# Kernel optimization log

Measured on AMD Instinct MI355X. Metric: run time of the kernel, lower is better.

The kernel has to match this reference:

```python
import jax, jax.numpy as jnp
import numpy as np

LN_EPS = 1e-5
NEG_INF = -1e30


def setup_inputs() -> dict:
    key = jax.random.key(0)
    ks = jax.random.split(key, 8)
    B, S, D_MODEL, Q_IN = 1, 2048, 1024, 512
    HI, DI = 16, 64            # indexer heads / head_dim
    H, DQK, DV = 8, 64, 64     # MLA heads, qk_head_dim, v_head_dim
    return {
        "x": jax.random.normal(ks[0], (B, S, D_MODEL), jnp.float32),
        "q_input": jax.random.normal(ks[1], (B, S, Q_IN), jnp.float32),
        "q": jax.random.normal(ks[2], (B, S, H, DQK), jnp.float32),
        "k": jax.random.normal(ks[3], (B, S, H, DQK), jnp.float32),
        "v": jax.random.normal(ks[4], (B, S, H, DV), jnp.float32),
        "w_q": jax.random.normal(ks[5], (Q_IN, HI * DI), jnp.float32) * (Q_IN ** -0.5),
        "w_k": jax.random.normal(ks[6], (D_MODEL, DI), jnp.float32) * (D_MODEL ** -0.5),
        "ln_g": jnp.ones((DI,), jnp.float32),
        "ln_b": jnp.zeros((DI,), jnp.float32),
        "w_weights": jax.random.normal(ks[7], (D_MODEL, HI), jnp.float32) * (D_MODEL ** -0.5),
        "top_k": 128,
    }


def _indexer_topk(x, q_input, w_q, w_k, ln_g, ln_b, w_weights, top_k):
    """Lightning indexer: per-head relevance scores -> weighted sum -> causal top-k indices."""
    B, S, _ = x.shape
    HI = w_weights.shape[1]
    DI = w_k.shape[1]
    qi = (q_input @ w_q).reshape(B, S, HI, DI)          # bqhd
    ki = x @ w_k                                         # bkd
    mu = ki.mean(-1, keepdims=True)
    var = ((ki - mu) ** 2).mean(-1, keepdims=True)
    ki = (ki - mu) * jax.lax.rsqrt(var + LN_EPS) * ln_g + ln_b
    # per-head weights; scores*w summed over h == (sum_h w*q) . k  (fused, same math)
    w = (x @ w_weights) * (HI ** -0.5)                   # bqh
    q_eff = jnp.einsum("bqhd,bqh->bqd", qi, w) * (DI ** -0.5)
    scores = jnp.einsum("bqd,bkd->bqk", q_eff, ki)       # [B,S,S]
    pos = jnp.arange(S)
    causal = jnp.where(pos[None, :] <= pos[:, None], 0.0, NEG_INF).astype(scores.dtype)
    scores = scores + causal[None]
    return jax.lax.top_k(scores, top_k)[1]               # [B,S,K]


def reference(x, q_input, q, k, v, w_q, w_k, ln_g, ln_b, w_weights, top_k):
    B, S, H, DQK = q.shape
    DV = v.shape[-1]
    idx = _indexer_topk(x, q_input, w_q, w_k, ln_g, ln_b, w_weights, top_k)  # [B,S,K]

    qh = q.transpose(0, 2, 1, 3)   # [B,H,Sq,D]
    kh = k.transpose(0, 2, 1, 3)   # [B,H,Sk,D]
    vh = v.transpose(0, 2, 1, 3)

    def gather(kv, ix):            # kv [Sk,D], ix [Sq,K] -> [Sq,K,D]
        return kv[ix]

    gather_h = jax.vmap(gather, in_axes=(0, None))       # over heads, shared idx
    gather_bh = jax.vmap(gather_h, in_axes=(0, 0))       # over batch
    k_sel = gather_bh(kh, idx)     # [B,H,Sq,K,D]
    v_sel = gather_bh(vh, idx)     # [B,H,Sq,K,Dv]

    att = jnp.einsum("bhqd,bhqkd->bhqk", qh, k_sel) * (DQK ** -0.5)
    pos = jnp.arange(S)
    valid = idx[:, None, :, :] <= pos[None, None, :, None]   # causal validity of gathered idx
    att = jnp.where(valid, att, NEG_INF)
    p = jax.nn.softmax(att, axis=-1)
    out = jnp.einsum("bhqk,bhqkd->bhqd", p, v_sel)
    return out.transpose(0, 2, 1, 3)   # [B,S,H,Dv]
```

## Files before the change

### kernel.cpp

```cpp
#include <hip/hip_runtime.h>
#include <hip/hip_bf16.h>
#include <hip/hip_fp16.h>
#include <math.h>

#define S 2048
#define DM 1024
#define QIN 512
#define HI 16
#define DI 64
#define NH 8
#define TOPK 128
#define LN_EPS 1e-5f
#define KP 8

typedef float f32x4 __attribute__((ext_vector_type(4)));
typedef short s16x8 __attribute__((ext_vector_type(8)));

__device__ __forceinline__ float wave_sum(float v){
#pragma unroll
  for (int o = 32; o; o >>= 1) v += __shfl_xor(v, o);
  return v;
}
__device__ __forceinline__ float wave_max(float v){
#pragma unroll
  for (int o = 32; o; o >>= 1) v = fmaxf(v, __shfl_xor(v, o));
  return v;
}
__device__ __forceinline__ unsigned short f2bf(float x){
  unsigned u = __float_as_uint(x);
  unsigned r = u + 0x7FFFu + ((u >> 16) & 1u);
  return (unsigned short)(r >> 16);
}
__device__ __forceinline__ float bf2f(unsigned short s){
  return __uint_as_float(((unsigned)s) << 16);
}
__device__ __forceinline__ unsigned short f2h(float x){
  return __half_as_ushort(__float2half_rn(x));
}
union UH2 { unsigned int u; __half2 h; };
__device__ __forceinline__ __half2 as_half2(unsigned int u){ UH2 x; x.u = u; return x.h; }

__global__ __launch_bounds__(256) void k_prep(const float* __restrict__ qin,
                                              unsigned short* __restrict__ Ah,
                                              unsigned short* __restrict__ Al,
                                              const float* __restrict__ k,
                                              unsigned short* __restrict__ kh,
                                              const float* __restrict__ v,
                                              unsigned short* __restrict__ vh,
                                              const float* __restrict__ wq,
                                              unsigned short* __restrict__ Bh,
                                              unsigned short* __restrict__ Bl){
  __shared__ unsigned short lh[32][33];
  __shared__ unsigned short ll[32][33];
  const int SEG0 = S * QIN / 4;
  const int SEG1 = S * NH * 64 / 4;
  const int bid = blockIdx.x;
  if (bid < 3072){
    int id = bid * 256 + threadIdx.x;
    if (id < SEG0){
      float4 f = ((const float4*)qin)[id];
      ushort4 h, lo;
      h.x = f2bf(f.x); lo.x = f2bf(f.x - bf2f(h.x));
      h.y = f2bf(f.y); lo.y = f2bf(f.y - bf2f(h.y));
      h.z = f2bf(f.z); lo.z = f2bf(f.z - bf2f(h.z));
      h.w = f2bf(f.w); lo.w = f2bf(f.w - bf2f(h.w));
      ((ushort4*)Ah)[id] = h;
      ((ushort4*)Al)[id] = lo;
    } else if (id < SEG0 + SEG1){
      int j = id - SEG0;
      float4 f = ((const float4*)k)[j];
      ushort4 o;
      o.x = f2h(f.x); o.y = f2h(f.y); o.z = f2h(f.z); o.w = f2h(f.w);
      ((ushort4*)kh)[j] = o;
    } else {
      int j = id - SEG0 - SEG1;
      float4 f = ((const float4*)v)[j];
      ushort4 o;
      o.x = f2h(f.x); o.y = f2h(f.y); o.z = f2h(f.z); o.w = f2h(f.w);
      ((ushort4*)vh)[j] = o;
    }
    return;
  }
  const int b2 = bid - 3072;
  const int k0 = (b2 & 15) * 32;
  const int n0 = (b2 >> 4) * 32;
  const int t = threadIdx.x;
  const int c = t & 31, r8 = t >> 5;
#pragma unroll
  for (int i = 0; i < 4; ++i){
    int kk = r8 + i * 8;
    float wv = wq[(size_t)(k0 + kk) * 1024 + n0 + c];
    unsigned short h = f2bf(wv);
    lh[c][kk] = h;
    ll[c][kk] = f2bf(wv - bf2f(h));
  }
  __syncthreads();
  const int kk = t & 31, nl = t >> 5;
#pragma unroll
  for (int i = 0; i < 4; ++i){
    int nn = nl + i * 8;
    Bh[(size_t)(n0 + nn) * QIN + k0 + kk] = lh[nn][kk];
    Bl[(size_t)(n0 + nn) * QIN + k0 + kk] = ll[nn][kk];
  }
}

__global__ __launch_bounds__(256) void k_part(const float* __restrict__ x,
                                              const float* __restrict__ wk,
                                              const float* __restrict__ ww,
                                              float* __restrict__ part){
  const int kp = blockIdx.x;
  const int bm = blockIdx.y;
  const int t  = threadIdx.x;
  const int m0 = bm * 64;
  __shared__ float As[32][68];
  __shared__ float Bs[32][84];
  const int tm = (t & 15) * 4;
  const int tn = (t >> 4) * 5;
  float acc[4][5];
#pragma unroll
  for (int i = 0; i < 4; i++)
#pragma unroll
    for (int j = 0; j < 5; j++) acc[i][j] = 0.f;

  for (int kb = 0; kb < (DM / KP) / 32; ++kb){
    const int k0 = kp * (DM / KP) + kb * 32;
#pragma unroll
    for (int i = 0; i < 2; i++){
      int u = t + i * 256;
      int m = u >> 3, c4 = u & 7;
      float4 a = *(const float4*)&x[(size_t)(m0 + m) * DM + k0 + c4 * 4];
      As[c4*4+0][m] = a.x; As[c4*4+1][m] = a.y; As[c4*4+2][m] = a.z; As[c4*4+3][m] = a.w;
    }
#pragma unroll
    for (int i = 0; i < 10; i++){
      int u = t + i * 256;
      int kk = u / 80, nn = u % 80;
      float val = (nn < 64) ? wk[(size_t)(k0 + kk) * 64 + nn]
                            : ww[(size_t)(k0 + kk) * 16 + (nn - 64)];
      Bs[kk][nn] = val;
    }
    __syncthreads();
#pragma unroll
    for (int k = 0; k < 32; ++k){
      float4 a = *(const float4*)&As[k][tm];
      float av[4] = {a.x, a.y, a.z, a.w};
      float bb[5];
#pragma unroll
      for (int j = 0; j < 5; j++) bb[j] = Bs[k][tn + j];
#pragma unroll
      for (int i = 0; i < 4; i++)
#pragma unroll
        for (int j = 0; j < 5; j++) acc[i][j] = fmaf(av[i], bb[j], acc[i][j]);
    }
    __syncthreads();
  }
  float* dst = part + (size_t)kp * S * 80;
#pragma unroll
  for (int i = 0; i < 4; i++)
#pragma unroll
    for (int j = 0; j < 5; j++)
      dst[(size_t)(m0 + tm + i) * 80 + tn + j] = acc[i][j];
}

__global__ __launch_bounds__(256) void k_lnw(const float* __restrict__ part,
                                             const float* __restrict__ g,
                                             const float* __restrict__ b,
                                             float* __restrict__ ki,
                                             float* __restrict__ wgt){
  const int s = blockIdx.x * 4 + (threadIdx.x >> 6);
  const int l = threadIdx.x & 63;
  float kv = 0.f;
#pragma unroll
  for (int p = 0; p < KP; p++) kv += part[(size_t)p * S * 80 + (size_t)s * 80 + l];
  float wv = 0.f;
  if (l < 16){
#pragma unroll
    for (int p = 0; p < KP; p++) wv += part[(size_t)p * S * 80 + (size_t)s * 80 + 64 + l];
  }
  float mu = wave_sum(kv) * (1.f / 64.f);
  float d  = kv - mu;
  float var = wave_sum(d * d) * (1.f / 64.f);
  float o = d * (1.f / sqrtf(var + LN_EPS)) * g[l] + b[l];
  ki[(size_t)s * 64 + l] = o;
  if (l < 16) wgt[(size_t)s * 16 + l] = wv * 0.25f;
}

__global__ __launch_bounds__(256) void k_qi_mfma(const unsigned short* __restrict__ Ah,
                                                 const unsigned short* __restrict__ Al,
                                                 const unsigned short* __restrict__ Bh,
                                                 const unsigned short* __restrict__ Bl,
                                                 float* __restrict__ qi){
  const int bn = blockIdx.x;
  const int bm = blockIdx.y;
  const int w = threadIdx.x >> 6, l = threadIdx.x & 63;
  const int m0 = bm * 64 + (w >> 1) * 32;
  const int n0 = bn * 64 + (w & 1) * 32;
  const int r = l & 15, kg = l >> 4;

  f32x4 acc00 = {0,0,0,0}, acc01 = {0,0,0,0}, acc10 = {0,0,0,0}, acc11 = {0,0,0,0};

  const size_t aoff = (size_t)(m0 + r) * QIN + kg * 8;
  const size_t boff = (size_t)(n0 + r) * QIN + kg * 8;
#pragma unroll 4
  for (int k0 = 0; k0 < QIN; k0 += 32){
    s16x8 ah0 = *(const s16x8*)(Ah + aoff + k0);
    s16x8 ah1 = *(const s16x8*)(Ah + aoff + 16 * QIN + k0);
    s16x8 al0 = *(const s16x8*)(Al + aoff + k0);
    s16x8 al1 = *(const s16x8*)(Al + aoff + 16 * QIN + k0);
    s16x8 bh0 = *(const s16x8*)(Bh + boff + k0);
    s16x8 bh1 = *(const s16x8*)(Bh + boff + 16 * QIN + k0);
    s16x8 bl0 = *(const s16x8*)(Bl + boff + k0);
    s16x8 bl1 = *(const s16x8*)(Bl + boff + 16 * QIN + k0);
    acc00 = __builtin_amdgcn_mfma_f32_16x16x32_bf16(ah0, bh0, acc00, 0, 0, 0);
    acc00 = __builtin_amdgcn_mfma_f32_16x16x32_bf16(ah0, bl0, acc00, 0, 0, 0);
    acc00 = __builtin_amdgcn_mfma_f32_16x16x32_bf16(al0, bh0, acc00, 0, 0, 0);
    acc01 = __builtin_amdgcn_mfma_f32_16x16x32_bf16(ah0, bh1, acc01, 0, 0, 0);
    acc01 = __builtin_amdgcn_mfma_f32_16x16x32_bf16(ah0, bl1, acc01, 0, 0, 0);
    acc01 = __builtin_amdgcn_mfma_f32_16x16x32_bf16(al0, bh1, acc01, 0, 0, 0);
    acc10 = __builtin_amdgcn_mfma_f32_16x16x32_bf16(ah1, bh0, acc10, 0, 0, 0);
    acc10 = __builtin_amdgcn_mfma_f32_16x16x32_bf16(ah1, bl0, acc10, 0, 0, 0);
    acc10 = __builtin_amdgcn_mfma_f32_16x16x32_bf16(al1, bh0, acc10, 0, 0, 0);
    acc11 = __builtin_amdgcn_mfma_f32_16x16x32_bf16(ah1, bh1, acc11, 0, 0, 0);
    acc11 = __builtin_amdgcn_mfma_f32_16x16x32_bf16(ah1, bl1, acc11, 0, 0, 0);
    acc11 = __builtin_amdgcn_mfma_f32_16x16x32_bf16(al1, bh1, acc11, 0, 0, 0);
  }
#pragma unroll
  for (int j = 0; j < 4; ++j){
    qi[(size_t)(m0 +  0 + kg * 4 + j) * 1024 + n0 +  0 + r] = acc00[j];
    qi[(size_t)(m0 +  0 + kg * 4 + j) * 1024 + n0 + 16 + r] = acc01[j];
    qi[(size_t)(m0 + 16 + kg * 4 + j) * 1024 + n0 +  0 + r] = acc10[j];
    qi[(size_t)(m0 + 16 + kg * 4 + j) * 1024 + n0 + 16 + r] = acc11[j];
  }
}

__global__ __launch_bounds__(256) void k_qeff(const float* __restrict__ qi,
                                              const float* __restrict__ wgt,
                                              float* __restrict__ qe){
  const int id = blockIdx.x * 256 + threadIdx.x;
  const int s = id >> 6, d = id & 63;
  float acc = 0.f;
#pragma unroll
  for (int h = 0; h < 16; h++)
    acc = fmaf(wgt[(size_t)s * 16 + h], qi[(size_t)s * 1024 + h * 64 + d], acc);
  qe[(size_t)s * 64 + d] = acc * 0.125f;
}

__global__ __launch_bounds__(256) void k_scores(const float* __restrict__ qe,
                                                const float* __restrict__ ki,
                                                float* __restrict__ sc){
  const int bj = blockIdx.x, bi = blockIdx.y;
  if (bj > bi) return;
  const int t = threadIdx.x;
  const int i0 = bi * 64, j0 = bj * 64;
  __shared__ float Qs[64][68];
  __shared__ float Ks[64][68];
#pragma unroll
  for (int u0 = 0; u0 < 4; ++u0){
    int u = t + u0 * 256;
    int r = u >> 4, d4 = u & 15;
    float4 a = *(const float4*)&qe[(size_t)(i0 + r) * 64 + d4 * 4];
    Qs[d4*4+0][r] = a.x; Qs[d4*4+1][r] = a.y; Qs[d4*4+2][r] = a.z; Qs[d4*4+3][r] = a.w;
    float4 b = *(const float4*)&ki[(size_t)(j0 + r) * 64 + d4 * 4];
    Ks[d4*4+0][r] = b.x; Ks[d4*4+1][r] = b.y; Ks[d4*4+2][r] = b.z; Ks[d4*4+3][r] = b.w;
  }
  __syncthreads();
  const int tm = (t & 15) * 4, tn = (t >> 4) * 4;
  float acc[4][4] = {};
#pragma unroll
  for (int d = 0; d < 64; ++d){
    float4 a = *(const float4*)&Qs[d][tm];
    float4 b = *(const float4*)&Ks[d][tn];
    float av[4] = {a.x, a.y, a.z, a.w}, bb[4] = {b.x, b.y, b.z, b.w};
#pragma unroll
    for (int i = 0; i < 4; i++)
#pragma unroll
      for (int j = 0; j < 4; j++) acc[i][j] = fmaf(av[i], bb[j], acc[i][j]);
  }
#pragma unroll
  for (int i = 0; i < 4; i++)
#pragma unroll
    for (int j = 0; j < 4; j++)
      sc[(size_t)(i0 + tm + i) * S + j0 + tn + j] = acc[i][j];
}

__global__ __launch_bounds__(256) void k_topk(const float* __restrict__ sc,
                                              int* __restrict__ idx,
                                              int* __restrict__ cnt){
  const int i = blockIdx.x, t = threadIdx.x;
  const int w = t >> 6, l = t & 63;
  const int n = i + 1;
  int* outr = idx + (size_t)i * TOPK;
  if (n <= TOPK){
    for (int m = t; m < n; m += 256) outr[m] = m;
    if (t == 0) cnt[i] = n;
    return;
  }
  __shared__ unsigned int keys[S];
  __shared__ int lA[S];
  __shared__ int lB[S];
  __shared__ int hist[256];
  __shared__ int wtot[4];
  __shared__ int s_b, s_above, s_out, s_m;
  hist[t] = 0;
  if (t == 0) s_out = 0;
  __syncthreads();
  for (int j = t; j < n; j += 256){
    unsigned int u = __float_as_uint(sc[(size_t)i * S + j]);
    unsigned int kk = (u & 0x80000000u) ? ~u : (u | 0x80000000u);
    keys[j] = kk;
    atomicAdd(&hist[kk >> 24], 1);
  }
  __syncthreads();
  int rem = TOPK;
  {
    const int h = hist[t];
    int vsc = h;
#pragma unroll
    for (int off = 1; off < 64; off <<= 1){
      int u = __shfl_down(vsc, off);
      if (l + off < 64) vsc += u;
    }
    if (l == 0) wtot[w] = vsc;
    __syncthreads();
    int later = 0;
#pragma unroll
    for (int ww = 1; ww < 4; ++ww) if (ww > w) later += wtot[ww];
    const int excl = vsc + later - h;
    if (excl < rem && excl + h >= rem){ s_b = t; s_above = excl; }
    __syncthreads();
  }
  int b = s_b;
  rem -= s_above;
  if (t == 0) s_m = 0;
  __syncthreads();
  for (int j = t; j < n; j += 256){
    int by = keys[j] >> 24;
    if (by > b){ int p = atomicAdd(&s_out, 1); outr[p] = j; }
    else if (by == b){ int p = atomicAdd(&s_m, 1); lA[p] = j; }
  }
  __syncthreads();
  int m = s_m;
  int* Lsrc = lA; int* Ldst = lB;
  bool done = false;
  if (m == rem){
    int base = TOPK - rem;
    for (int u = t; u < m; u += 256) outr[base + u] = Lsrc[u];
    done = true;
  }
  for (int p = 2; p >= 0 && !done; --p){
    const int sh = p * 8;
    __syncthreads();
    hist[t] = 0;
    __syncthreads();
    for (int u = t; u < m; u += 256) atomicAdd(&hist[(keys[Lsrc[u]] >> sh) & 255], 1);
    __syncthreads();
    {
      const int h = hist[t];
      int vsc = h;
#pragma unroll
      for (int off = 1; off < 64; off <<= 1){
        int u = __shfl_down(vsc, off);
        if (l + off < 64) vsc += u;
      }
      if (l == 0) wtot[w] = vsc;
      __syncthreads();
      int later = 0;
#pragma unroll
      for (int ww = 1; ww < 4; ++ww) if (ww > w) later += wtot[ww];
      const int excl = vsc + later - h;
      if (excl < rem && excl + h >= rem){ s_b = t; s_above = excl; }
      __syncthreads();
    }
    b = s_b;
    rem -= s_above;
    if (t == 0) s_m = 0;
    __syncthreads();
    for (int u = t; u < m; u += 256){
      int j = Lsrc[u]; int by = (keys[j] >> sh) & 255;
      if (by > b){ int p2 = atomicAdd(&s_out, 1); outr[p2] = j; }
      else if (by == b){ int p2 = atomicAdd(&s_m, 1); Ldst[p2] = j; }
    }
    __syncthreads();
    m = s_m;
    { int* tmp = Lsrc; Lsrc = Ldst; Ldst = tmp; }
    if (m == rem){
      int base = TOPK - rem;
      for (int u = t; u < m; u += 256) outr[base + u] = Lsrc[u];
      done = true;
    }
  }
  if (!done && t == 0){
    int base = TOPK - rem;
    for (int a = 0; a < rem; ++a){
      int mn = 1 << 30, pos = -1;
      for (int u = 0; u < m; ++u){ int j = Lsrc[u]; if (j < mn){ mn = j; pos = u; } }
      outr[base + a] = mn; Lsrc[pos] = 1 << 30;
    }
  }
  if (t == 0) cnt[i] = TOPK;
}

__global__ __launch_bounds__(256) void k_attn(const float* __restrict__ q,
                                              const unsigned short* __restrict__ kh,
                                              const unsigned short* __restrict__ vh,
                                              const int* __restrict__ idx,
                                              const int* __restrict__ cnt,
                                              float* __restrict__ out){
  const int i = blockIdx.x;
  const int w = threadIdx.x >> 6, l = threadIdx.x & 63;
  const int n = cnt[i];
  const int* irow = idx + (size_t)i * TOPK;

  __shared__ int   sidx[4][TOPK];
  __shared__ float sp[4][2][TOPK];

  sidx[w][l]      = (l < n)      ? irow[l]      : 0;
  sidx[w][l + 64] = (l + 64 < n) ? irow[l + 64] : 0;

  const int h0 = 2 * w, h1 = h0 + 1;
  const int g = l >> 3, gl = l & 7;
  const float* qrow = q + (size_t)i * (NH * 64);
  __half2 qa2[4], qb2[4];
  {
    float4 a0 = *(const float4*)&qrow[h0 * 64 + gl * 8];
    float4 a1 = *(const float4*)&qrow[h0 * 64 + gl * 8 + 4];
    float4 b0 = *(const float4*)&qrow[h1 * 64 + gl * 8];
    float4 b1 = *(const float4*)&qrow[h1 * 64 + gl * 8 + 4];
    qa2[0] = __floats2half2_rn(a0.x * 0.125f, a0.y * 0.125f);
    qa2[1] = __floats2half2_rn(a0.z * 0.125f, a0.w * 0.125f);
    qa2[2] = __floats2half2_rn(a1.x * 0.125f, a1.y * 0.125f);
    qa2[3] = __floats2half2_rn(a1.z * 0.125f, a1.w * 0.125f);
    qb2[0] = __floats2half2_rn(b0.x * 0.125f, b0.y * 0.125f);
    qb2[1] = __floats2half2_rn(b0.z * 0.125f, b0.w * 0.125f);
    qb2[2] = __floats2half2_rn(b1.x * 0.125f, b1.y * 0.125f);
    qb2[3] = __floats2half2_rn(b1.z * 0.125f, b1.w * 0.125f);
  }
  asm volatile("" ::: "memory");

#pragma unroll 4
  for (int pass = 0; pass < TOPK / 8; ++pass){
    const int j = pass * 8 + g;
    const size_t base = (size_t)sidx[w][j] * (NH * 64);
    uint4 u0 = *(const uint4*)(kh + base + h0 * 64 + gl * 8);
    uint4 u1 = *(const uint4*)(kh + base + h1 * 64 + gl * 8);
    __half2 acc0 = __floats2half2_rn(0.f, 0.f);
    __half2 acc1 = __floats2half2_rn(0.f, 0.f);
    acc0 = __hfma2(as_half2(u0.x), qa2[0], acc0);
    acc0 = __hfma2(as_half2(u0.y), qa2[1], acc0);
    acc0 = __hfma2(as_half2(u0.z), qa2[2], acc0);
    acc0 = __hfma2(as_half2(u0.w), qa2[3], acc0);
    acc1 = __hfma2(as_half2(u1.x), qb2[0], acc1);
    acc1 = __hfma2(as_half2(u1.y), qb2[1], acc1);
    acc1 = __hfma2(as_half2(u1.z), qb2[2], acc1);
    acc1 = __hfma2(as_half2(u1.w), qb2[3], acc1);
    float d0 = __low2float(acc0) + __high2float(acc0);
    float d1 = __low2float(acc1) + __high2float(acc1);
#pragma unroll
    for (int o = 1; o < 8; o <<= 1){ d0 += __shfl_xor(d0, o); d1 += __shfl_xor(d1, o); }
    if (gl == 0){ sp[w][0][j] = d0; sp[w][1][j] = d1; }
  }
  asm volatile("" ::: "memory");

  const bool v0 = (l < n), v1 = (l + 64 < n);
  {
    float s0 = v0 ? sp[w][0][l] : -1e30f, s1 = v1 ? sp[w][0][l + 64] : -1e30f;
    float m = wave_max(fmaxf(s0, s1));
    float e0 = v0 ? __expf(s0 - m) : 0.f;
    float e1 = v1 ? __expf(s1 - m) : 0.f;
    float inv = 1.f / wave_sum(e0 + e1);
    sp[w][0][l] = e0 * inv;
    sp[w][0][l + 64] = e1 * inv;
  }
  {
    float s0 = v0 ? sp[w][1][l] : -1e30f, s1 = v1 ? sp[w][1][l + 64] : -1e30f;
    float m = wave_max(fmaxf(s0, s1));
    float e0 = v0 ? __expf(s0 - m) : 0.f;
    float e1 = v1 ? __expf(s1 - m) : 0.f;
    float inv = 1.f / wave_sum(e0 + e1);
    sp[w][1][l] = e0 * inv;
    sp[w][1][l + 64] = e1 * inv;
  }
  asm volatile("" ::: "memory");

  const int j2 = l >> 5;
  const int hp = (l >> 4) & 1;
  const int hh = h0 + hp;
  const int g4 = l & 15;
  float o4[4] = {0.f, 0.f, 0.f, 0.f};
#pragma unroll 4
  for (int pass = 0; pass < TOPK / 2; ++pass){
    const int j = pass * 2 + j2;
    const size_t base = (size_t)sidx[w][j] * (NH * 64);
    uint2 uv = *(const uint2*)(vh + base + hh * 64 + g4 * 4);
    __half2 v01 = as_half2(uv.x), v23 = as_half2(uv.y);
    float p = sp[w][hp][j];
    o4[0] = fmaf(p, __low2float(v01),  o4[0]);
    o4[1] = fmaf(p, __high2float(v01), o4[1]);
    o4[2] = fmaf(p, __low2float(v23),  o4[2]);
    o4[3] = fmaf(p, __high2float(v23), o4[3]);
  }
#pragma unroll
  for (int e = 0; e < 4; ++e) o4[e] += __shfl_xor(o4[e], 32);
  if (l < 32)
    *(float4*)&out[((size_t)i * NH + hh) * 64 + g4 * 4] = make_float4(o4[0], o4[1], o4[2], o4[3]);
}

extern "C" void kernel_launch(void* const* d_in, const int* in_sizes, int n_in,
                              void* d_out, int out_size, void* d_ws, size_t ws_size,
                              hipStream_t stream){
  const float* x   = (const float*)d_in[0];
  const float* qin = (const float*)d_in[1];
  const float* q   = (const float*)d_in[2];
  const float* k   = (const float*)d_in[3];
  const float* v   = (const float*)d_in[4];
  const float* wq  = (const float*)d_in[5];
  const float* wk  = (const float*)d_in[6];
  const float* lng = (const float*)d_in[7];
  const float* lnb = (const float*)d_in[8];
  const float* ww  = (const float*)d_in[9];
  float* out = (float*)d_out;

  float* ws   = (float*)d_ws;
  float* part = ws;
  float* ki   = ws + 1310720;
  float* wgt  = ws + 1441792;
  float* qi   = ws + 1474560;
  float* qe   = ws + 3571712;
  float* sc   = ws + 3702784;
  int*   idx  = (int*)(ws + 7897088);
  int*   cnt  = (int*)(ws + 8159232);
  unsigned short* kh = (unsigned short*)part;
  unsigned short* vh = kh + (size_t)S * NH * 64;
  unsigned short* Ah = (unsigned short*)sc;
  unsigned short* Al = Ah + (size_t)S * QIN;
  unsigned short* Bh = Al + (size_t)S * QIN;
  unsigned short* Bl = Bh + (size_t)1024 * QIN;

  hipLaunchKernelGGL(k_part,    dim3(KP, 32), dim3(256), 0, stream, x, wk, ww, part);
  hipLaunchKernelGGL(k_lnw,     dim3(512),    dim3(256), 0, stream, part, lng, lnb, ki, wgt);
  hipLaunchKernelGGL(k_prep,    dim3(3584),   dim3(256), 0, stream, qin, Ah, Al, k, kh, v, vh, wq, Bh, Bl);
  hipLaunchKernelGGL(k_qi_mfma, dim3(16, 32), dim3(256), 0, stream, Ah, Al, Bh, Bl, qi);
  hipLaunchKernelGGL(k_qeff,    dim3(512),    dim3(256), 0, stream, qi, wgt, qe);
  hipLaunchKernelGGL(k_scores,  dim3(32, 32), dim3(256), 0, stream, qe, ki, sc);
  hipLaunchKernelGGL(k_topk,    dim3(2048),   dim3(256), 0, stream, sc, idx, cnt);
  hipLaunchKernelGGL(k_attn,    dim3(2048),   dim3(256), 0, stream, q, kh, vh, idx, cnt, out);
}
```

Before: 120.1 us.

## Merge independent prep kernels into two launches and widen V gather loads

```diff
diff --git a/kernel.cpp b/kernel.cpp
--- a/kernel.cpp
+++ b/kernel.cpp
@@ -40,23 +40,82 @@
 union UH2 { unsigned int u; __half2 h; };
 __device__ __forceinline__ __half2 as_half2(unsigned int u){ UH2 x; x.u = u; return x.h; }
 
-__global__ __launch_bounds__(256) void k_prep(const float* __restrict__ qin,
-                                              unsigned short* __restrict__ Ah,
-                                              unsigned short* __restrict__ Al,
-                                              const float* __restrict__ k,
-                                              unsigned short* __restrict__ kh,
-                                              const float* __restrict__ v,
-                                              unsigned short* __restrict__ vh,
-                                              const float* __restrict__ wq,
-                                              unsigned short* __restrict__ Bh,
-                                              unsigned short* __restrict__ Bl){
-  __shared__ unsigned short lh[32][33];
-  __shared__ unsigned short ll[32][33];
-  const int SEG0 = S * QIN / 4;
-  const int SEG1 = S * NH * 64 / 4;
+__global__ __launch_bounds__(256) void k_f1(const float* __restrict__ x,
+                                            const float* __restrict__ wk,
+                                            const float* __restrict__ ww,
+                                            float* __restrict__ part,
+                                            const float* __restrict__ qin,
+                                            unsigned short* __restrict__ Ah,
+                                            unsigned short* __restrict__ Al,
+                                            const float* __restrict__ k,
+                                            unsigned short* __restrict__ kh,
+                                            const float* __restrict__ v,
+                                            unsigned short* __restrict__ vh,
+                                            const float* __restrict__ wq,
+                                            unsigned short* __restrict__ Bh,
+                                            unsigned short* __restrict__ Bl){
+  __shared__ float As[32][68];
+  __shared__ float Bs[32][84];
   const int bid = blockIdx.x;
-  if (bid < 3072){
-    int id = bid * 256 + threadIdx.x;
+  const int t = threadIdx.x;
+
+  if (bid < 256){
+    const int kp = bid & 7;
+    const int bm = bid >> 3;
+    const int m0 = bm * 64;
+    const int tm = (t & 15) * 4;
+    const int tn = (t >> 4) * 5;
+    float acc[4][5];
+#pragma unroll
+    for (int i = 0; i < 4; i++)
+#pragma unroll
+      for (int j = 0; j < 5; j++) acc[i][j] = 0.f;
+
+    for (int kb = 0; kb < (DM / KP) / 32; ++kb){
+      const int k0 = kp * (DM / KP) + kb * 32;
+#pragma unroll
+      for (int i = 0; i < 2; i++){
+        int u = t + i * 256;
+        int m = u >> 3, c4 = u & 7;
+        float4 a = *(const float4*)&x[(size_t)(m0 + m) * DM + k0 + c4 * 4];
+        As[c4*4+0][m] = a.x; As[c4*4+1][m] = a.y; As[c4*4+2][m] = a.z; As[c4*4+3][m] = a.w;
+      }
+#pragma unroll
+      for (int i = 0; i < 10; i++){
+        int u = t + i * 256;
+        int kk = u / 80, nn = u % 80;
+        float val = (nn < 64) ? wk[(size_t)(k0 + kk) * 64 + nn]
+                              : ww[(size_t)(k0 + kk) * 16 + (nn - 64)];
+        Bs[kk][nn] = val;
+      }
+      __syncthreads();
+#pragma unroll
+      for (int kk = 0; kk < 32; ++kk){
+        float4 a = *(const float4*)&As[kk][tm];
+        float av[4] = {a.x, a.y, a.z, a.w};
+        float bb[5];
+#pragma unroll
+        for (int j = 0; j < 5; j++) bb[j] = Bs[kk][tn + j];
+#pragma unroll
+        for (int i = 0; i < 4; i++)
+#pragma unroll
+          for (int j = 0; j < 5; j++) acc[i][j] = fmaf(av[i], bb[j], acc[i][j]);
+      }
+      __syncthreads();
+    }
+    float* dst = part + (size_t)kp * S * 80;
+#pragma unroll
+    for (int i = 0; i < 4; i++)
+#pragma unroll
+      for (int j = 0; j < 5; j++)
+        dst[(size_t)(m0 + tm + i) * 80 + tn + j] = acc[i][j];
+    return;
+  }
+
+  if (bid < 256 + 3072){
+    const int SEG0 = S * QIN / 4;
+    const int SEG1 = S * NH * 64 / 4;
+    int id = (bid - 256) * 256 + t;
     if (id < SEG0){
       float4 f = ((const float4*)qin)[id];
       ushort4 h, lo;
@@ -81,117 +140,66 @@
     }
     return;
   }
-  const int b2 = bid - 3072;
-  const int k0 = (b2 & 15) * 32;
-  const int n0 = (b2 >> 4) * 32;
-  const int t = threadIdx.x;
-  const int c = t & 31, r8 = t >> 5;
-#pragma unroll
-  for (int i = 0; i < 4; ++i){
-    int kk = r8 + i * 8;
-    float wv = wq[(size_t)(k0 + kk) * 1024 + n0 + c];
-    unsigned short h = f2bf(wv);
-    lh[c][kk] = h;
-    ll[c][kk] = f2bf(wv - bf2f(h));
-  }
-  __syncthreads();
-  const int kk = t & 31, nl = t >> 5;
-#pragma unroll
-  for (int i = 0; i < 4; ++i){
-    int nn = nl + i * 8;
-    Bh[(size_t)(n0 + nn) * QIN + k0 + kk] = lh[nn][kk];
-    Bl[(size_t)(n0 + nn) * QIN + k0 + kk] = ll[nn][kk];
-  }
-}
-
-__global__ __launch_bounds__(256) void k_part(const float* __restrict__ x,
-                                              const float* __restrict__ wk,
-                                              const float* __restrict__ ww,
-                                              float* __restrict__ part){
-  const int kp = blockIdx.x;
-  const int bm = blockIdx.y;
-  const int t  = threadIdx.x;
-  const int m0 = bm * 64;
-  __shared__ float As[32][68];
-  __shared__ float Bs[32][84];
-  const int tm = (t & 15) * 4;
-  const int tn = (t >> 4) * 5;
-  float acc[4][5];
-#pragma unroll
-  for (int i = 0; i < 4; i++)
-#pragma unroll
-    for (int j = 0; j < 5; j++) acc[i][j] = 0.f;
-
-  for (int kb = 0; kb < (DM / KP) / 32; ++kb){
-    const int k0 = kp * (DM / KP) + kb * 32;
-#pragma unroll
-    for (int i = 0; i < 2; i++){
-      int u = t + i * 256;
-      int m = u >> 3, c4 = u & 7;
-      float4 a = *(const float4*)&x[(size_t)(m0 + m) * DM + k0 + c4 * 4];
-      As[c4*4+0][m] = a.x; As[c4*4+1][m] = a.y; As[c4*4+2][m] = a.z; As[c4*4+3][m] = a.w;
-    }
-#pragma unroll
-    for (int i = 0; i < 10; i++){
-      int u = t + i * 256;
-      int kk = u / 80, nn = u % 80;
-      float val = (nn < 64) ? wk[(size_t)(k0 + kk) * 64 + nn]
-                            : ww[(size_t)(k0 + kk) * 16 + (nn - 64)];
-      Bs[kk][nn] = val;
-    }
-    __syncthreads();
-#pragma unroll
-    for (int k = 0; k < 32; ++k){
-      float4 a = *(const float4*)&As[k][tm];
-      float av[4] = {a.x, a.y, a.z, a.w};
-      float bb[5];
-#pragma unroll
-      for (int j = 0; j < 5; j++) bb[j] = Bs[k][tn + j];
-#pragma unroll
-      for (int i = 0; i < 4; i++)
-#pragma unroll
-        for (int j = 0; j < 5; j++) acc[i][j] = fmaf(av[i], bb[j], acc[i][j]);
-    }
-    __syncthreads();
-  }
-  float* dst = part + (size_t)kp * S * 80;
-#pragma unroll
-  for (int i = 0; i < 4; i++)
-#pragma unroll
-    for (int j = 0; j < 5; j++)
-      dst[(size_t)(m0 + tm + i) * 80 + tn + j] = acc[i][j];
-}
-
-__global__ __launch_bounds__(256) void k_lnw(const float* __restrict__ part,
-                                             const float* __restrict__ g,
-                                             const float* __restrict__ b,
-                                             float* __restrict__ ki,
-                                             float* __restrict__ wgt){
-  const int s = blockIdx.x * 4 + (threadIdx.x >> 6);
-  const int l = threadIdx.x & 63;
-  float kv = 0.f;
-#pragma unroll
-  for (int p = 0; p < KP; p++) kv += part[(size_t)p * S * 80 + (size_t)s * 80 + l];
-  float wv = 0.f;
-  if (l < 16){
-#pragma unroll
-    for (int p = 0; p < KP; p++) wv += part[(size_t)p * S * 80 + (size_t)s * 80 + 64 + l];
-  }
-  float mu = wave_sum(kv) * (1.f / 64.f);
-  float d  = kv - mu;
-  float var = wave_sum(d * d) * (1.f / 64.f);
-  float o = d * (1.f / sqrtf(var + LN_EPS)) * g[l] + b[l];
-  ki[(size_t)s * 64 + l] = o;
-  if (l < 16) wgt[(size_t)s * 16 + l] = wv * 0.25f;
-}
-
-__global__ __launch_bounds__(256) void k_qi_mfma(const unsigned short* __restrict__ Ah,
-                                                 const unsigned short* __restrict__ Al,
-                                                 const unsigned short* __restrict__ Bh,
-                                                 const unsigned short* __restrict__ Bl,
-                                                 float* __restrict__ qi){
-  const int bn = blockIdx.x;
-  const int bm = blockIdx.y;
+
+  {
+    unsigned short (*lh)[33] = (unsigned short(*)[33])&As[0][0];
+    unsigned short (*ll)[33] = (unsigned short(*)[33])&Bs[0][0];
+    const int b2 = bid - 3328;
+    const int k0 = (b2 & 15) * 32;
+    const int n0 = (b2 >> 4) * 32;
+    const int c = t & 31, r8 = t >> 5;
+#pragma unroll
+    for (int i = 0; i < 4; ++i){
+      int kk = r8 + i * 8;
+      float wv = wq[(size_t)(k0 + kk) * 1024 + n0 + c];
+      unsigned short h = f2bf(wv);
+      lh[c][kk] = h;
+      ll[c][kk] = f2bf(wv - bf2f(h));
+    }
+    __syncthreads();
+    const int kk = t & 31, nl = t >> 5;
+#pragma unroll
+    for (int i = 0; i < 4; ++i){
+      int nn = nl + i * 8;
+      Bh[(size_t)(n0 + nn) * QIN + k0 + kk] = lh[nn][kk];
+      Bl[(size_t)(n0 + nn) * QIN + k0 + kk] = ll[nn][kk];
+    }
+  }
+}
+
+__global__ __launch_bounds__(256) void k_f2(const float* __restrict__ part,
+                                            const float* __restrict__ g,
+                                            const float* __restrict__ b,
+                                            float* __restrict__ ki,
+                                            float* __restrict__ wgt,
+                                            const unsigned short* __restrict__ Ah,
+                                            const unsigned short* __restrict__ Al,
+                                            const unsigned short* __restrict__ Bh,
+                                            const unsigned short* __restrict__ Bl,
+                                            float* __restrict__ qi){
+  const int bid = blockIdx.x;
+  if (bid < 512){
+    const int s = bid * 4 + (threadIdx.x >> 6);
+    const int l = threadIdx.x & 63;
+    float kv = 0.f;
+#pragma unroll
+    for (int p = 0; p < KP; p++) kv += part[(size_t)p * S * 80 + (size_t)s * 80 + l];
+    float wv = 0.f;
+    if (l < 16){
+#pragma unroll
+      for (int p = 0; p < KP; p++) wv += part[(size_t)p * S * 80 + (size_t)s * 80 + 64 + l];
+    }
+    float mu = wave_sum(kv) * (1.f / 64.f);
+    float d  = kv - mu;
+    float var = wave_sum(d * d) * (1.f / 64.f);
+    float o = d * (1.f / sqrtf(var + LN_EPS)) * g[l] + b[l];
+    ki[(size_t)s * 64 + l] = o;
+    if (l < 16) wgt[(size_t)s * 16 + l] = wv * 0.25f;
+    return;
+  }
+  const int b2 = bid - 512;
+  const int bn = b2 & 15;
+  const int bm = b2 >> 4;
   const int w = threadIdx.x >> 6, l = threadIdx.x & 63;
   const int m0 = bm * 64 + (w >> 1) * 32;
   const int n0 = bn * 64 + (w & 1) * 32;
@@ -482,27 +490,36 @@
   }
   asm volatile("" ::: "memory");
 
-  const int j2 = l >> 5;
-  const int hp = (l >> 4) & 1;
-  const int hh = h0 + hp;
-  const int g4 = l & 15;
-  float o4[4] = {0.f, 0.f, 0.f, 0.f};
+  const int kq = l >> 4;
+  const int hp = (l >> 3) & 1;
+  const int d8 = (l & 7) * 8;
+  float o8[8] = {0,0,0,0,0,0,0,0};
 #pragma unroll 4
-  for (int pass = 0; pass < TOPK / 2; ++pass){
-    const int j = pass * 2 + j2;
+  for (int pass = 0; pass < TOPK / 4; ++pass){
+    const int j = pass * 4 + kq;
     const size_t base = (size_t)sidx[w][j] * (NH * 64);
-    uint2 uv = *(const uint2*)(vh + base + hh * 64 + g4 * 4);
-    __half2 v01 = as_half2(uv.x), v23 = as_half2(uv.y);
+    uint4 uv = *(const uint4*)(vh + base + (h0 + hp) * 64 + d8);
     float p = sp[w][hp][j];
-    o4[0] = fmaf(p, __low2float(v01),  o4[0]);
-    o4[1] = fmaf(p, __high2float(v01), o4[1]);
-    o4[2] = fmaf(p, __low2float(v23),  o4[2]);
-    o4[3] = fmaf(p, __high2float(v23), o4[3]);
-  }
-#pragma unroll
-  for (int e = 0; e < 4; ++e) o4[e] += __shfl_xor(o4[e], 32);
-  if (l < 32)
-    *(float4*)&out[((size_t)i * NH + hh) * 64 + g4 * 4] = make_float4(o4[0], o4[1], o4[2], o4[3]);
+    __half2 va = as_half2(uv.x), vb = as_half2(uv.y), vc = as_half2(uv.z), vd = as_half2(uv.w);
+    o8[0] = fmaf(p, __low2float(va),  o8[0]);
+    o8[1] = fmaf(p, __high2float(va), o8[1]);
+    o8[2] = fmaf(p, __low2float(vb),  o8[2]);
+    o8[3] = fmaf(p, __high2float(vb), o8[3]);
+    o8[4] = fmaf(p, __low2float(vc),  o8[4]);
+    o8[5] = fmaf(p, __high2float(vc), o8[5]);
+    o8[6] = fmaf(p, __low2float(vd),  o8[6]);
+    o8[7] = fmaf(p, __high2float(vd), o8[7]);
+  }
+#pragma unroll
+  for (int e = 0; e < 8; ++e){
+    o8[e] += __shfl_xor(o8[e], 16);
+    o8[e] += __shfl_xor(o8[e], 32);
+  }
+  if (l < 16){
+    float* dst = &out[(size_t)i * (NH * 64) + (h0 + hp) * 64 + d8];
+    *(float4*)dst       = make_float4(o8[0], o8[1], o8[2], o8[3]);
+    *(float4*)(dst + 4) = make_float4(o8[4], o8[5], o8[6], o8[7]);
+  }
 }
 
 extern "C" void kernel_launch(void* const* d_in, const int* in_sizes, int n_in,
@@ -529,19 +546,19 @@
   float* sc   = ws + 3702784;
   int*   idx  = (int*)(ws + 7897088);
   int*   cnt  = (int*)(ws + 8159232);
-  unsigned short* kh = (unsigned short*)part;
+  unsigned short* kh = (unsigned short*)(ws + 8161280);
   unsigned short* vh = kh + (size_t)S * NH * 64;
   unsigned short* Ah = (unsigned short*)sc;
   unsigned short* Al = Ah + (size_t)S * QIN;
   unsigned short* Bh = Al + (size_t)S * QIN;
   unsigned short* Bl = Bh + (size_t)1024 * QIN;
 
-  hipLaunchKernelGGL(k_part,    dim3(KP, 32), dim3(256), 0, stream, x, wk, ww, part);
-  hipLaunchKernelGGL(k_lnw,     dim3(512),    dim3(256), 0, stream, part, lng, lnb, ki, wgt);
-  hipLaunchKernelGGL(k_prep,    dim3(3584),   dim3(256), 0, stream, qin, Ah, Al, k, kh, v, vh, wq, Bh, Bl);
-  hipLaunchKernelGGL(k_qi_mfma, dim3(16, 32), dim3(256), 0, stream, Ah, Al, Bh, Bl, qi);
-  hipLaunchKernelGGL(k_qeff,    dim3(512),    dim3(256), 0, stream, qi, wgt, qe);
-  hipLaunchKernelGGL(k_scores,  dim3(32, 32), dim3(256), 0, stream, qe, ki, sc);
-  hipLaunchKernelGGL(k_topk,    dim3(2048),   dim3(256), 0, stream, sc, idx, cnt);
-  hipLaunchKernelGGL(k_attn,    dim3(2048),   dim3(256), 0, stream, q, kh, vh, idx, cnt, out);
-}
+  hipLaunchKernelGGL(k_f1,     dim3(3840),   dim3(256), 0, stream,
+                     x, wk, ww, part, qin, Ah, Al, k, kh, v, vh, wq, Bh, Bl);
+  hipLaunchKernelGGL(k_f2,     dim3(1024),   dim3(256), 0, stream,
+                     part, lng, lnb, ki, wgt, Ah, Al, Bh, Bl, qi);
+  hipLaunchKernelGGL(k_qeff,   dim3(512),    dim3(256), 0, stream, qi, wgt, qe);
+  hipLaunchKernelGGL(k_scores, dim3(32, 32), dim3(256), 0, stream, qe, ki, sc);
+  hipLaunchKernelGGL(k_topk,   dim3(2048),   dim3(256), 0, stream, sc, idx, cnt);
+  hipLaunchKernelGGL(k_attn,   dim3(2048),   dim3(256), 0, stream, q, kh, vh, idx, cnt, out);
+}
```

Result: faster. 113.7 us (-5.4%).
